# Kernel optimization log

Hardware: AMD Instinct MI355X
Metric: run time of the kernel (lower is better)

The kernel has to match this reference:

```python
import jax, jax.numpy as jnp
import numpy as np

N_SRC = 50000
N_DST = 50000
N_EDGES = 1600000
D_IN = 128
K = 8          # num_heads
D_OUT = 16     # out_dim per head (K*D_OUT = 128)
NEG_SLOPE = 0.2


def setup_inputs() -> dict:
    key = jax.random.key(0)
    ks = jax.random.split(key, 8)
    feat_src = jax.random.normal(ks[0], (N_SRC, D_IN), dtype=jnp.float32)
    feat_dst = jax.random.normal(ks[1], (N_DST, D_IN), dtype=jnp.float32)
    W_src = jax.random.normal(ks[2], (D_IN, K * D_OUT), dtype=jnp.float32) * (1.0 / np.sqrt(D_IN))
    b_src = jnp.zeros((K * D_OUT,), dtype=jnp.float32)
    W_dst = jax.random.normal(ks[3], (D_IN, K * D_OUT), dtype=jnp.float32) * (1.0 / np.sqrt(D_IN))
    b_dst = jnp.zeros((K * D_OUT,), dtype=jnp.float32)
    attn_src = jax.random.normal(ks[4], (K, 2 * D_OUT), dtype=jnp.float32) * 0.1
    src_idx = jax.random.randint(ks[5], (N_EDGES,), 0, N_SRC, dtype=jnp.int64)
    dst_idx = jax.random.randint(ks[6], (N_EDGES,), 0, N_DST, dtype=jnp.int64)
    return {"feat_src": feat_src, "feat_dst": feat_dst, "W_src": W_src, "b_src": b_src,
            "W_dst": W_dst, "b_dst": b_dst, "attn_src": attn_src,
            "src_idx": src_idx, "dst_idx": dst_idx}


def reference(feat_src, feat_dst, W_src, b_src, W_dst, b_dst, attn_src, src_idx, dst_idx):
    n_dst = feat_dst.shape[0]
    # feat_drop is identity (p=0). Linear projections, reshape to heads.
    hs = (feat_src @ W_src + b_src).reshape(-1, K, D_OUT)  # [N_src, K, D_out]
    hd = (feat_dst @ W_dst + b_dst).reshape(-1, K, D_OUT)  # [N_dst, K, D_out]
    # per-node attention logits
    el = jnp.sum(hs * attn_src[:, :D_OUT], axis=-1)  # [N_src, K]
    er = jnp.sum(hd * attn_src[:, D_OUT:], axis=-1)  # [N_dst, K]
    # per-edge score: u_add_v then LeakyReLU
    e = el[src_idx] + er[dst_idx]                    # [E, K]
    e = jnp.where(e >= 0, e, NEG_SLOPE * e)
    # edge softmax over incoming edges of each dst node (numerically stable)
    emax = jax.ops.segment_max(e, dst_idx, num_segments=n_dst)
    emax = jnp.where(jnp.isfinite(emax), emax, 0.0)  # handle dsts with no edges
    ee = jnp.exp(e - emax[dst_idx])                  # [E, K]
    esum = jax.ops.segment_sum(ee, dst_idx, num_segments=n_dst)
    a = ee / esum[dst_idx]                           # [E, K]
    # weighted message aggregation: u_mul_e then sum over incoming edges
    m = hs[src_idx] * a[:, :, None]                  # [E, K, D_out]
    out = jax.ops.segment_sum(m, dst_idx, num_segments=n_dst)  # [N_dst, K, D_out]
    return out.reshape(n_dst, K * D_OUT)
```

## Files before the change

### kernel.cpp

```cpp
#include <hip/hip_runtime.h>
#include <hip/hip_bf16.h>

#define NEG_SLOPE 0.2f
#define LOG2E 1.4426950408889634f
#define EPB   8192
#define BINSZ 32
#define CAP   2048
#define MAXC  2048

#if defined(__has_builtin) && __has_builtin(__builtin_amdgcn_exp2f)
#define EXP2F(x) __builtin_amdgcn_exp2f(x)
#else
#define EXP2F(x) exp2f(x)
#endif

typedef __attribute__((ext_vector_type(8))) short bf16x8;
typedef __attribute__((ext_vector_type(4))) float f32x4;

__device__ __forceinline__ float b2f_lo(unsigned u) { return __uint_as_float(u << 16); }
__device__ __forceinline__ float b2f_hi(unsigned u) { return __uint_as_float(u & 0xffff0000u); }

__device__ __forceinline__ short f2b(float x) {
    unsigned u = __float_as_uint(x);
    unsigned r = (u + 0x7fffu + ((u >> 16) & 1u)) >> 16;
    return (short)r;
}

__global__ __launch_bounds__(256) void pack_kernel(
    const float* __restrict__ W_src, const float* __restrict__ W_dst,
    const float* __restrict__ b_src, const float* __restrict__ b_dst,
    const float* __restrict__ attn,
    uint4* __restrict__ wp_src, uint4* __restrict__ wp_dst,
    float* __restrict__ c_all,
    int* __restrict__ cursor, int nCoarse)
{
    const int e = blockIdx.x * 256 + threadIdx.x;
    if (e < 4608) {
        const int which = e / 2304;
        const int e2 = e % 2304;
        const float* W = which ? W_dst : W_src;
        uint4* wp = which ? wp_dst : wp_src;
        const int aoff = which ? 16 : 0;
        short out[8];
        if (e2 < 2048) {
            const int t = e2 >> 8, q = (e2 >> 6) & 3, l = e2 & 63;
            const int kbase = (l >> 4) * 8 + q * 32;
            const int n = t * 16 + (l & 15);
            #pragma unroll
            for (int j = 0; j < 8; ++j) out[j] = f2b(W[(size_t)(kbase + j) * 128 + n]);
            *(uint4*)&wp[(t * 4 + q) * 64 + l] = *(uint4*)out;
        } else {
            const int e3 = e2 - 2048;
            const int q = e3 >> 6, l = e3 & 63;
            const int kbase = (l >> 4) * 8 + q * 32;
            const int n = l & 15;
            #pragma unroll
            for (int j = 0; j < 8; ++j) {
                float v = 0.f;
                if (n < 8) {
                    for (int dd = 0; dd < 16; ++dd)
                        v += W[(size_t)(kbase + j) * 128 + n * 16 + dd] * attn[n * 32 + aoff + dd];
                }
                out[j] = f2b(v);
            }
            *(uint4*)&wp[(32 + q) * 64 + l] = *(uint4*)out;
        }
    } else if (e < 4624) {
        const int k = e - 4608;
        const int which = k >> 3, kk = k & 7;
        const float* bb = which ? b_dst : b_src;
        const int aoff = which ? 16 : 0;
        float v = 0.f;
        for (int dd = 0; dd < 16; ++dd) v += bb[kk * 16 + dd] * attn[kk * 32 + aoff + dd];
        c_all[k] = v;
    } else if (e < 4624 + nCoarse) {
        const int c = e - 4624;
        cursor[c] = c * CAP;
    }
}

__device__ __forceinline__ void scatter_body(
    const int* __restrict__ src_idx, const int* __restrict__ dst_idx,
    int* __restrict__ cursor, int* __restrict__ coarse,
    int nEdges, int nCoarse, int bx)
{
    __shared__ int lcnt[MAXC];
    __shared__ int lbase[MAXC];
    const int t = threadIdx.x;
    for (int i = t; i < nCoarse; i += 256) lcnt[i] = 0;
    __syncthreads();
    const int e0 = bx * EPB;
    const int e1 = min(e0 + EPB, nEdges);
    for (int e = e0 + t; e < e1; e += 256) atomicAdd(&lcnt[dst_idx[e] >> 5], 1);
    __syncthreads();
    for (int i = t; i < nCoarse; i += 256) {
        const int c = lcnt[i];
        lbase[i] = c ? atomicAdd(&cursor[i], c) : 0;
        lcnt[i] = 0;
    }
    __syncthreads();
    for (int e = e0 + t; e < e1; e += 256) {
        const int d = dst_idx[e];
        const int s = src_idx[e];
        const int bin = d >> 5;
        const int lr = atomicAdd(&lcnt[bin], 1);
        const int pos = lbase[bin] + lr;
        if (pos < (bin + 1) * CAP)
            coarse[pos] = (s << 5) | (d & 31);
    }
}

template<bool STORE_H>
__device__ __forceinline__ void proj_body(
    const float* __restrict__ feat, const uint4* __restrict__ wp,
    const float* __restrict__ b, const float* __restrict__ cvec,
    short* __restrict__ hs_out, float* __restrict__ el_out,
    int N, int bx)
{
    const int t = threadIdx.x;
    const int lane = t & 63;
    const int w = t >> 6;
    const int m  = lane & 15;
    const int q8 = lane >> 4;
    const int row0 = bx * 128 + w * 32;

    f32x4 acc0[9], acc1[9];
    #pragma unroll
    for (int tt = 0; tt < 8; ++tt) {
        const float bn = b[tt * 16 + m];
        acc0[tt] = (f32x4){bn, bn, bn, bn};
        acc1[tt] = (f32x4){bn, bn, bn, bn};
    }
    acc0[8] = (f32x4){0.f, 0.f, 0.f, 0.f};
    acc1[8] = (f32x4){0.f, 0.f, 0.f, 0.f};

    int rowA0 = row0 + m;      if (rowA0 >= N) rowA0 = N - 1;
    int rowA1 = row0 + 16 + m; if (rowA1 >= N) rowA1 = N - 1;
    const float* f0 = feat + (size_t)rowA0 * 128 + q8 * 8;
    const float* f1 = feat + (size_t)rowA1 * 128 + q8 * 8;
    const bf16x8* wpv = (const bf16x8*)wp;

    #pragma unroll
    for (int kc = 0; kc < 4; ++kc) {
        const float4 fa0 = *(const float4*)(f0 + kc * 32);
        const float4 fb0 = *(const float4*)(f0 + kc * 32 + 4);
        const float4 fa1 = *(const float4*)(f1 + kc * 32);
        const float4 fb1 = *(const float4*)(f1 + kc * 32 + 4);
        bf16x8 a0, a1;
        a0[0]=f2b(fa0.x); a0[1]=f2b(fa0.y); a0[2]=f2b(fa0.z); a0[3]=f2b(fa0.w);
        a0[4]=f2b(fb0.x); a0[5]=f2b(fb0.y); a0[6]=f2b(fb0.z); a0[7]=f2b(fb0.w);
        a1[0]=f2b(fa1.x); a1[1]=f2b(fa1.y); a1[2]=f2b(fa1.z); a1[3]=f2b(fa1.w);
        a1[4]=f2b(fb1.x); a1[5]=f2b(fb1.y); a1[6]=f2b(fb1.z); a1[7]=f2b(fb1.w);
        #pragma unroll
        for (int tt = 0; tt < 8; ++tt) {
            const bf16x8 bf = wpv[(tt * 4 + kc) * 64 + lane];
            acc0[tt] = __builtin_amdgcn_mfma_f32_16x16x32_bf16(a0, bf, acc0[tt], 0, 0, 0);
            acc1[tt] = __builtin_amdgcn_mfma_f32_16x16x32_bf16(a1, bf, acc1[tt], 0, 0, 0);
        }
        {
            const bf16x8 bv = wpv[(32 + kc) * 64 + lane];
            acc0[8] = __builtin_amdgcn_mfma_f32_16x16x32_bf16(a0, bv, acc0[8], 0, 0, 0);
            acc1[8] = __builtin_amdgcn_mfma_f32_16x16x32_bf16(a1, bv, acc1[8], 0, 0, 0);
        }
    }

    #pragma unroll
    for (int half = 0; half < 2; ++half) {
        const f32x4* acc = half ? acc1 : acc0;
        const int rbase = row0 + half * 16 + q8 * 4;
        #pragma unroll
        for (int reg = 0; reg < 4; ++reg) {
            const int row = rbase + reg;
            if (row < N) {
                if (STORE_H) {
                    #pragma unroll
                    for (int tt = 0; tt < 8; ++tt)
                        hs_out[(size_t)row * 128 + tt * 16 + m] = f2b(acc[tt][reg]);
                }
                if (m < 8) el_out[(size_t)row * 8 + m] = (acc[8][reg] + cvec[m]) * LOG2E;
            }
        }
    }
}

__global__ __launch_bounds__(256, 2) void fused_kernel(
    const float* __restrict__ feat_src, const float* __restrict__ feat_dst,
    const uint4* __restrict__ wp_src, const uint4* __restrict__ wp_dst,
    const float* __restrict__ b_src, const float* __restrict__ b_dst,
    const float* __restrict__ c_all,
    short* __restrict__ hs, float* __restrict__ el, float* __restrict__ er,
    const int* __restrict__ src_idx, const int* __restrict__ dst_idx,
    int* __restrict__ cursor, int* __restrict__ coarse,
    int n_src, int n_dst, int nEdges, int nCoarse, int nSB, int pSrcBlocks)
{
    int bx = blockIdx.x;
    if (bx < nSB) { scatter_body(src_idx, dst_idx, cursor, coarse, nEdges, nCoarse, bx); return; }
    bx -= nSB;
    if (bx < pSrcBlocks) {
        proj_body<true>(feat_src, wp_src, b_src, c_all, hs, el, n_src, bx);
        return;
    }
    bx -= pSrcBlocks;
    proj_body<false>(feat_dst, wp_dst, b_dst, c_all + 8, nullptr, er, n_dst, bx);
}

__global__ __launch_bounds__(256, 8) void sort_reduce_kernel(
    const int* __restrict__ coarse, const int* __restrict__ cursor,
    const float* __restrict__ el,
    const float* __restrict__ er,
    const unsigned short* __restrict__ hs,
    float* __restrict__ out,
    int n_dst, int nCoarse)
{
    __shared__ int fpk[CAP];
    __shared__ int h[BINSZ];
    __shared__ int lbeg[BINSZ];
    __shared__ int cu[BINSZ];
    __shared__ float erL[BINSZ * 8];
    const int t = threadIdx.x, c = blockIdx.x;
    const int base_in = c * CAP;
    const int cnt = min(cursor[c] - base_in, CAP);

    {
        const int d = c * BINSZ + (t >> 3);
        erL[t] = (d < n_dst) ? er[(size_t)d * 8 + (t & 7)] : 0.f;
    }
    if (t < BINSZ) h[t] = 0;
    __syncthreads();

    int ev[8];
    #pragma unroll
    for (int r = 0; r < 8; ++r) {
        const int idx = t + (r << 8);
        ev[r] = (idx < cnt) ? coarse[base_in + idx] : -1;
    }
    #pragma unroll
    for (int r = 0; r < 8; ++r)
        if (ev[r] >= 0) atomicAdd(&h[ev[r] & 31], 1);
    __syncthreads();
    if (t < BINSZ) {
        const int v = h[t];
        int sc = v;
        #pragma unroll
        for (int off = 1; off < BINSZ; off <<= 1) {
            const int nb = __shfl_up(sc, off);
            if (t >= off) sc += nb;
        }
        lbeg[t] = sc - v;
        cu[t]   = sc - v;
    }
    __syncthreads();
    #pragma unroll
    for (int r = 0; r < 8; ++r)
        if (ev[r] >= 0) {
            const int p = atomicAdd(&cu[ev[r] & 31], 1);
            fpk[p] = ev[r];
        }
    __syncthreads();

    const int w = t >> 6, lane = t & 63;
    const int sub = lane >> 5;
    const int l32 = lane & 31;
    const int k   = l32 >> 2;
    const uint2* hs2 = (const uint2*)hs;
    for (int j = 0; j < 8; ++j) {
        const int dl = w * 8 + j;
        const int d  = c * BINSZ + dl;
        if (d >= n_dst) break;
        const float erk = erL[dl * 8 + k];
        const int beg = lbeg[dl], end = lbeg[dl] + h[dl];
        float a0 = 0.f, a1 = 0.f, a2 = 0.f, a3 = 0.f, es = 0.f;

        int i  = beg + sub;
        float lA = 0.f; uint2 uA = make_uint2(0u, 0u);
        if (i < end) {
            const int sA = fpk[i] >> 5;
            lA = el[(size_t)sA * 8 + k];
            uA = hs2[(size_t)sA * 32 + l32];
        }
        int i2 = i + 2;
        int sB = (i2 < end) ? (fpk[i2] >> 5) : 0;
        while (i < end) {
            const int i3 = i2 + 2;
            float lB = 0.f; uint2 uB = uA;
            if (i2 < end) {
                lB = el[(size_t)sB * 8 + k];
                uB = hs2[(size_t)sB * 32 + l32];
            }
            const int sC = (i3 < end) ? (fpk[i3] >> 5) : 0;
            float x = lA + erk; x = (x >= 0.f) ? x : NEG_SLOPE * x;
            const float ee = EXP2F(x);
            es += ee;
            a0 = fmaf(ee, b2f_lo(uA.x), a0); a1 = fmaf(ee, b2f_hi(uA.x), a1);
            a2 = fmaf(ee, b2f_lo(uA.y), a2); a3 = fmaf(ee, b2f_hi(uA.y), a3);
            i = i2; i2 = i3; sB = sC; lA = lB; uA = uB;
        }

        es += __shfl_xor(es, 32);
        a0 += __shfl_xor(a0, 32);
        a1 += __shfl_xor(a1, 32);
        a2 += __shfl_xor(a2, 32);
        a3 += __shfl_xor(a3, 32);
        if (sub == 0) {
            const float inv = (es > 0.f) ? 1.f / es : 0.f;
            float4 o;
            o.x = a0 * inv; o.y = a1 * inv; o.z = a2 * inv; o.w = a3 * inv;
            *(float4*)(out + (size_t)d * 128 + l32 * 4) = o;
        }
    }
}

extern "C" void kernel_launch(void* const* d_in, const int* in_sizes, int n_in,
                              void* d_out, int out_size, void* d_ws, size_t ws_size,
                              hipStream_t stream) {
    const float* feat_src = (const float*)d_in[0];
    const float* feat_dst = (const float*)d_in[1];
    const float* W_src    = (const float*)d_in[2];
    const float* b_src    = (const float*)d_in[3];
    const float* W_dst    = (const float*)d_in[4];
    const float* b_dst    = (const float*)d_in[5];
    const float* attn     = (const float*)d_in[6];
    const int*   src_idx  = (const int*)d_in[7];
    const int*   dst_idx  = (const int*)d_in[8];
    float* out = (float*)d_out;

    const int n_src  = in_sizes[0] / 128;
    const int n_dst  = in_sizes[1] / 128;
    const int nEdges = in_sizes[7];

    const int nCoarse = (n_dst + BINSZ - 1) / BINSZ;
    const int nSB     = (nEdges + EPB - 1) / EPB;
    const int pSrc    = (n_src + 127) / 128;
    const int pDst    = (n_dst + 127) / 128;

    unsigned short* hs = (unsigned short*)d_ws;
    float* el = (float*)(hs + (size_t)n_src * 128);
    float* er = el + (size_t)n_src * 8;
    int* cursor = (int*)(er + (size_t)n_dst * 8);
    uintptr_t p = (uintptr_t)(cursor + nCoarse);
    p = (p + 15) & ~(uintptr_t)15;
    int* coarse = (int*)p;
    uintptr_t p2 = (uintptr_t)(coarse + (size_t)nCoarse * CAP);
    p2 = (p2 + 15) & ~(uintptr_t)15;
    uint4* wp_src = (uint4*)p2;
    uint4* wp_dst = wp_src + 36 * 64;
    float* c_all  = (float*)(wp_dst + 36 * 64);

    const int packBlocks = (4624 + nCoarse + 255) / 256;
    pack_kernel<<<packBlocks, 256, 0, stream>>>(W_src, W_dst, b_src, b_dst, attn,
                                                wp_src, wp_dst, c_all, cursor, nCoarse);

    fused_kernel<<<nSB + pSrc + pDst, 256, 0, stream>>>(
        feat_src, feat_dst, wp_src, wp_dst, b_src, b_dst, c_all,
        (short*)hs, el, er, src_idx, dst_idx, cursor, coarse,
        n_src, n_dst, nEdges, nCoarse, nSB, pSrc);

    sort_reduce_kernel<<<nCoarse, 256, 0, stream>>>(coarse, cursor, el, er,
                                                    hs, out, n_dst, nCoarse);
}
```

Baseline: 232.9 us.

## Gather 16-byte bf16 rows with four edge groups per wave and packed FMAs

Restructures the aggregation loop so each wave processes four edges at a time, with 16 lanes per edge each loading 16 bytes (8 bf16 values) instead of 32 lanes loading 8 bytes. The manual software-pipelined prefetch is dropped in favour of a simple strided loop, and the accumulation uses 2-wide float vectors so the compiler can emit packed FMAs. The intent is to widen memory transactions and raise memory-level parallelism per wave. The cost is an extra shuffle-reduction stage and more idle lanes at the tail for low-degree nodes (about 32 edges each).

```diff
diff --git a/kernel.cpp b/kernel.cpp
--- a/kernel.cpp
+++ b/kernel.cpp
@@ -16,6 +16,7 @@
 
 typedef __attribute__((ext_vector_type(8))) short bf16x8;
 typedef __attribute__((ext_vector_type(4))) float f32x4;
+typedef __attribute__((ext_vector_type(2))) float f32x2;
 
 __device__ __forceinline__ float b2f_lo(unsigned u) { return __uint_as_float(u << 16); }
 __device__ __forceinline__ float b2f_hi(unsigned u) { return __uint_as_float(u & 0xffff0000u); }
@@ -259,53 +260,50 @@
     __syncthreads();
 
     const int w = t >> 6, lane = t & 63;
-    const int sub = lane >> 5;
-    const int l32 = lane & 31;
-    const int k   = l32 >> 2;
-    const uint2* hs2 = (const uint2*)hs;
+    const int g   = lane >> 4;
+    const int l16 = lane & 15;
+    const int k   = l16 >> 1;
+    const uint4* hs4 = (const uint4*)hs;
     for (int j = 0; j < 8; ++j) {
         const int dl = w * 8 + j;
         const int d  = c * BINSZ + dl;
         if (d >= n_dst) break;
         const float erk = erL[dl * 8 + k];
         const int beg = lbeg[dl], end = lbeg[dl] + h[dl];
-        float a0 = 0.f, a1 = 0.f, a2 = 0.f, a3 = 0.f, es = 0.f;
-
-        int i  = beg + sub;
-        float lA = 0.f; uint2 uA = make_uint2(0u, 0u);
-        if (i < end) {
-            const int sA = fpk[i] >> 5;
-            lA = el[(size_t)sA * 8 + k];
-            uA = hs2[(size_t)sA * 32 + l32];
-        }
-        int i2 = i + 2;
-        int sB = (i2 < end) ? (fpk[i2] >> 5) : 0;
-        while (i < end) {
-            const int i3 = i2 + 2;
-            float lB = 0.f; uint2 uB = uA;
-            if (i2 < end) {
-                lB = el[(size_t)sB * 8 + k];
-                uB = hs2[(size_t)sB * 32 + l32];
-            }
-            const int sC = (i3 < end) ? (fpk[i3] >> 5) : 0;
-            float x = lA + erk; x = (x >= 0.f) ? x : NEG_SLOPE * x;
+        f32x2 a01 = (f32x2){0.f, 0.f}, a23 = (f32x2){0.f, 0.f};
+        f32x2 a45 = (f32x2){0.f, 0.f}, a67 = (f32x2){0.f, 0.f};
+        float es = 0.f;
+        for (int i = beg + g; i < end; i += 4) {
+            const int s = fpk[i] >> 5;
+            const float lg = el[(size_t)s * 8 + k];
+            const uint4 u = hs4[(size_t)s * 16 + l16];
+            float x = lg + erk; x = (x >= 0.f) ? x : NEG_SLOPE * x;
             const float ee = EXP2F(x);
             es += ee;
-            a0 = fmaf(ee, b2f_lo(uA.x), a0); a1 = fmaf(ee, b2f_hi(uA.x), a1);
-            a2 = fmaf(ee, b2f_lo(uA.y), a2); a3 = fmaf(ee, b2f_hi(uA.y), a3);
-            i = i2; i2 = i3; sB = sC; lA = lB; uA = uB;
-        }
-
-        es += __shfl_xor(es, 32);
-        a0 += __shfl_xor(a0, 32);
-        a1 += __shfl_xor(a1, 32);
-        a2 += __shfl_xor(a2, 32);
-        a3 += __shfl_xor(a3, 32);
-        if (sub == 0) {
+            a01 = (f32x2){b2f_lo(u.x), b2f_hi(u.x)} * ee + a01;
+            a23 = (f32x2){b2f_lo(u.y), b2f_hi(u.y)} * ee + a23;
+            a45 = (f32x2){b2f_lo(u.z), b2f_hi(u.z)} * ee + a45;
+            a67 = (f32x2){b2f_lo(u.w), b2f_hi(u.w)} * ee + a67;
+        }
+        float r0 = a01.x, r1 = a01.y, r2 = a23.x, r3 = a23.y;
+        float r4 = a45.x, r5 = a45.y, r6 = a67.x, r7 = a67.y;
+        es += __shfl_xor(es, 16); es += __shfl_xor(es, 32);
+        r0 += __shfl_xor(r0, 16); r0 += __shfl_xor(r0, 32);
+        r1 += __shfl_xor(r1, 16); r1 += __shfl_xor(r1, 32);
+        r2 += __shfl_xor(r2, 16); r2 += __shfl_xor(r2, 32);
+        r3 += __shfl_xor(r3, 16); r3 += __shfl_xor(r3, 32);
+        r4 += __shfl_xor(r4, 16); r4 += __shfl_xor(r4, 32);
+        r5 += __shfl_xor(r5, 16); r5 += __shfl_xor(r5, 32);
+        r6 += __shfl_xor(r6, 16); r6 += __shfl_xor(r6, 32);
+        r7 += __shfl_xor(r7, 16); r7 += __shfl_xor(r7, 32);
+        if (lane < 16) {
             const float inv = (es > 0.f) ? 1.f / es : 0.f;
-            float4 o;
-            o.x = a0 * inv; o.y = a1 * inv; o.z = a2 * inv; o.w = a3 * inv;
-            *(float4*)(out + (size_t)d * 128 + l32 * 4) = o;
+            float4 o1, o2;
+            o1.x = r0 * inv; o1.y = r1 * inv; o1.z = r2 * inv; o1.w = r3 * inv;
+            o2.x = r4 * inv; o2.y = r5 * inv; o2.z = r6 * inv; o2.w = r7 * inv;
+            float* op = out + (size_t)d * 128 + l16 * 8;
+            *(float4*)op = o1;
+            *(float4*)(op + 4) = o2;
         }
     }
 }
```

Result: faster. 226.1 us (-2.9%).
